# Performance work log

Measured on AMD Instinct MI355X. Metric: run time of the kernel, lower is better.

Reference implementation:

```python
import jax, jax.numpy as jnp
import numpy as np

C, B, D = 1_000_000, 4096, 128

def setup_inputs() -> dict:
    key = jax.random.key(0)
    ks = jax.random.split(key, 7)
    nodes = jax.random.normal(ks[0], (C, D), dtype=jnp.float32)
    z_local = jax.random.normal(ks[1], (B, D), dtype=jnp.float32)
    z_meta = jax.random.normal(ks[2], (D,), dtype=jnp.float32)
    # MLP params: Linear(3D -> D), GELU, Linear(D -> 1)
    W1 = jax.random.normal(ks[3], (3 * D, D), dtype=jnp.float32) / np.sqrt(3 * D)
    b1 = jnp.zeros((D,), dtype=jnp.float32)
    W2 = jax.random.normal(ks[4], (D, 1), dtype=jnp.float32) / np.sqrt(D)
    b2 = jnp.zeros((1,), dtype=jnp.float32)
    batch = jnp.sort(jax.random.randint(ks[5], (C,), 0, B, dtype=jnp.int64))
    return {"nodes": nodes, "z_local": z_local, "z_meta": z_meta,
            "W1": W1, "b1": b1, "W2": W2, "b2": b2, "batch": batch}

def reference(nodes, z_local, z_meta, W1, b1, W2, b2, batch):
    # gather per-graph global vector for each node, broadcast batch-wide meta
    z_local_tiled = z_local[batch]                       # [C, D]
    z_meta_tiled = jnp.broadcast_to(z_meta[None, :], nodes.shape)  # [C, D]
    combined = jnp.concatenate([nodes, z_local_tiled, z_meta_tiled], axis=-1)  # [C, 3D]
    h = jax.nn.gelu(combined @ W1 + b1, approximate=False)  # [C, D]
    logits = (h @ W2 + b2).squeeze(-1)                       # [C]
    return logits
```

## Files before the change

### kernel.cpp

```cpp
#include <hip/hip_runtime.h>
#include <hip/hip_bf16.h>


typedef __attribute__((ext_vector_type(8))) __bf16 bf16x8;
typedef __attribute__((ext_vector_type(4))) float f32x4;

#define D_DIM 128

__device__ __forceinline__ float gelu_exact(float x) {
    float t = 0.70710678118654752f * x;
    float a = fabsf(t);
    float d = __builtin_amdgcn_rcpf(fmaf(0.3275911f, a, 1.0f));
    float p = fmaf(1.061405429f, d, -1.453152027f);
    p = fmaf(p, d, 1.421413741f);
    p = fmaf(p, d, -0.284496736f);
    p = fmaf(p, d, 0.254829592f);
    p = p * d;
    float e = __builtin_amdgcn_exp2f(a * a * -1.4426950408889634f);
    float erf_a = fmaf(-p, e, 1.0f);
    float erf_t = copysignf(erf_a, t);
    return 0.5f * x * (1.0f + erf_t);
}

__global__ void prep_bias2(const float* __restrict__ z_meta, const float* __restrict__ W1,
                           const float* __restrict__ b1, float* __restrict__ bias2) {
    int n = threadIdx.x;
    float s = b1[n];
    for (int k = 0; k < D_DIM; ++k)
        s = fmaf(z_meta[k], W1[(2 * D_DIM + k) * D_DIM + n], s);
    bias2[n] = s;
}

__global__ void prep_w1f(const float* __restrict__ W1, __bf16* __restrict__ w1f) {
    int f = blockIdx.x * 256 + threadIdx.x;
    int j = f & 7, lane = (f >> 3) & 63, nt = (f >> 9) & 7, kc = f >> 12;
    int k = kc * 32 + (lane >> 4) * 8 + j;
    int n = nt * 16 + (lane & 15);
    w1f[f] = (__bf16)W1[k * D_DIM + n];
}

__global__ __launch_bounds__(128) void prep_pre(const float* __restrict__ z_local,
                                                const float* __restrict__ W1,
                                                const float* __restrict__ bias2,
                                                float* __restrict__ pre) {
    int n = threadIdx.x;
    int g0 = blockIdx.x * 8;
    float bz = bias2[n];
    float s[8];
#pragma unroll
    for (int g = 0; g < 8; ++g) s[g] = bz;
    for (int k = 0; k < D_DIM; ++k) {
        float wk = W1[(D_DIM + k) * D_DIM + n];
#pragma unroll
        for (int g = 0; g < 8; ++g)
            s[g] = fmaf(z_local[(size_t)(g0 + g) * D_DIM + k], wk, s[g]);
    }
#pragma unroll
    for (int g = 0; g < 8; ++g) pre[(size_t)(g0 + g) * D_DIM + n] = s[g];
}

__global__ __launch_bounds__(256) void readout_main(
    const float* __restrict__ nodes, const int* __restrict__ batch,
    const float* __restrict__ pre, const __bf16* __restrict__ w1f,
    const float* __restrict__ W2, const float* __restrict__ b2,
    float* __restrict__ out) {
    const int tid = threadIdx.x;
    const int wave = tid >> 6;
    const int lane = tid & 63;
    const int q = lane >> 4;
    const int c0 = lane & 15;
    const int row_base = blockIdx.x * 64 + wave * 16;

    const float* aptr = nodes + (size_t)(row_base + c0) * D_DIM + q * 8;
    f32x4 a[8];
#pragma unroll
    for (int kc = 0; kc < 4; ++kc) {
        a[2 * kc]     = *((const f32x4*)(aptr + kc * 32));
        a[2 * kc + 1] = *((const f32x4*)(aptr + kc * 32 + 4));
    }
    int brow[4];
#pragma unroll
    for (int r = 0; r < 4; ++r) brow[r] = batch[row_base + q * 4 + r];
    float w2v[8];
#pragma unroll
    for (int nt = 0; nt < 8; ++nt) w2v[nt] = W2[nt * 16 + c0];
    const float b2v = b2[0];

    f32x4 acc[8] = {};

    const bf16x8* bfr = (const bf16x8*)w1f;
#pragma unroll
    for (int kc = 0; kc < 4; ++kc) {
        bf16x8 af;
#pragma unroll
        for (int j = 0; j < 8; ++j)
            af[j] = (__bf16)a[2 * kc + (j >> 2)][j & 3];
#pragma unroll
        for (int nt = 0; nt < 8; ++nt) {
            bf16x8 bf = bfr[(kc * 8 + nt) * 64 + lane];
            acc[nt] = __builtin_amdgcn_mfma_f32_16x16x32_bf16(af, bf, acc[nt], 0, 0, 0);
        }
    }

#pragma unroll
    for (int r = 0; r < 4; ++r) {
        const float* prow = pre + (size_t)brow[r] * D_DIM;
        float partial = 0.f;
#pragma unroll
        for (int nt = 0; nt < 8; ++nt) {
            float u = acc[nt][r] + prow[nt * 16 + c0];
            partial += gelu_exact(u) * w2v[nt];
        }
        partial += __shfl_xor(partial, 1);
        partial += __shfl_xor(partial, 2);
        partial += __shfl_xor(partial, 4);
        partial += __shfl_xor(partial, 8);
        if (c0 == 0) out[row_base + q * 4 + r] = partial + b2v;
    }
}

extern "C" void kernel_launch(void* const* d_in, const int* in_sizes, int n_in,
                              void* d_out, int out_size, void* d_ws, size_t ws_size,
                              hipStream_t stream) {
    const float* nodes   = (const float*)d_in[0];
    const float* z_local = (const float*)d_in[1];
    const float* z_meta  = (const float*)d_in[2];
    const float* W1      = (const float*)d_in[3];
    const float* b1      = (const float*)d_in[4];
    const float* W2      = (const float*)d_in[5];
    const float* b2      = (const float*)d_in[6];
    const int*   batch   = (const int*)d_in[7];
    float* out = (float*)d_out;

    char* ws = (char*)d_ws;
    __bf16* w1f  = (__bf16*)ws;
    float* bias2 = (float*)(ws + 32768);
    float* pre   = (float*)(ws + 33280);

    prep_bias2<<<1, 128, 0, stream>>>(z_meta, W1, b1, bias2);
    prep_w1f<<<64, 256, 0, stream>>>(W1, w1f);
    prep_pre<<<512, 128, 0, stream>>>(z_local, W1, bias2, pre);

    readout_main<<<15625, 256, 0, stream>>>(nodes, batch, pre, w1f, W2, b2, out);
}
```

Baseline: 727.3 us.

## Fuse prep kernels into one launch and stage W1 fragments in LDS

Result: faster. 690.7 us (-5.0%).

```diff
diff --git a/kernel.cpp b/kernel.cpp
--- a/kernel.cpp
+++ b/kernel.cpp
@@ -1,9 +1,12 @@
 #include <hip/hip_runtime.h>
 #include <hip/hip_bf16.h>
+#include <cstdint>
 
 
 typedef __attribute__((ext_vector_type(8))) __bf16 bf16x8;
 typedef __attribute__((ext_vector_type(4))) float f32x4;
+typedef __attribute__((address_space(3))) uint32_t lds_u32;
+typedef __attribute__((address_space(1))) const uint32_t glob_u32;
 
 #define D_DIM 128
 
@@ -22,48 +25,48 @@
     return 0.5f * x * (1.0f + erf_t);
 }
 
-__global__ void prep_bias2(const float* __restrict__ z_meta, const float* __restrict__ W1,
-                           const float* __restrict__ b1, float* __restrict__ bias2) {
-    int n = threadIdx.x;
-    float s = b1[n];
-    for (int k = 0; k < D_DIM; ++k)
-        s = fmaf(z_meta[k], W1[(2 * D_DIM + k) * D_DIM + n], s);
-    bias2[n] = s;
-}
-
-__global__ void prep_w1f(const float* __restrict__ W1, __bf16* __restrict__ w1f) {
-    int f = blockIdx.x * 256 + threadIdx.x;
-    int j = f & 7, lane = (f >> 3) & 63, nt = (f >> 9) & 7, kc = f >> 12;
-    int k = kc * 32 + (lane >> 4) * 8 + j;
-    int n = nt * 16 + (lane & 15);
-    w1f[f] = (__bf16)W1[k * D_DIM + n];
-}
-
-__global__ __launch_bounds__(128) void prep_pre(const float* __restrict__ z_local,
-                                                const float* __restrict__ W1,
-                                                const float* __restrict__ bias2,
-                                                float* __restrict__ pre) {
-    int n = threadIdx.x;
-    int g0 = blockIdx.x * 8;
-    float bz = bias2[n];
-    float s[8];
+__global__ __launch_bounds__(256) void prep_all(
+    const float* __restrict__ z_local, const float* __restrict__ z_meta,
+    const float* __restrict__ W1, const float* __restrict__ b1,
+    __bf16* __restrict__ w1f, float* __restrict__ bias2, float* __restrict__ pre) {
+    const int blk = blockIdx.x;
+    const int tid = threadIdx.x;
+    if (blk < 64) {
+        int f = blk * 256 + tid;
+        int j = f & 7, lane = (f >> 3) & 63, nt = (f >> 9) & 7, kc = f >> 12;
+        int k = kc * 32 + (lane >> 4) * 8 + j;
+        int n = nt * 16 + (lane & 15);
+        w1f[f] = (__bf16)W1[k * D_DIM + n];
+    } else if (blk == 64) {
+        if (tid < D_DIM) {
+            int n = tid;
+            float s = b1[n];
+            for (int k = 0; k < D_DIM; ++k)
+                s = fmaf(z_meta[k], W1[(2 * D_DIM + k) * D_DIM + n], s);
+            bias2[n] = s;
+        }
+    } else {
+        int pb = blk - 65;
+        int n = tid & 127;
+        int g0 = pb * 8 + (tid >> 7) * 4;
+        float s[4] = {0.f, 0.f, 0.f, 0.f};
+        for (int k = 0; k < D_DIM; ++k) {
+            float wk = W1[(D_DIM + k) * D_DIM + n];
 #pragma unroll
-    for (int g = 0; g < 8; ++g) s[g] = bz;
-    for (int k = 0; k < D_DIM; ++k) {
-        float wk = W1[(D_DIM + k) * D_DIM + n];
+            for (int g = 0; g < 4; ++g)
+                s[g] = fmaf(z_local[(size_t)(g0 + g) * D_DIM + k], wk, s[g]);
+        }
 #pragma unroll
-        for (int g = 0; g < 8; ++g)
-            s[g] = fmaf(z_local[(size_t)(g0 + g) * D_DIM + k], wk, s[g]);
+        for (int g = 0; g < 4; ++g) pre[(size_t)(g0 + g) * D_DIM + n] = s[g];
     }
-#pragma unroll
-    for (int g = 0; g < 8; ++g) pre[(size_t)(g0 + g) * D_DIM + n] = s[g];
 }
 
 __global__ __launch_bounds__(256) void readout_main(
     const float* __restrict__ nodes, const int* __restrict__ batch,
     const float* __restrict__ pre, const __bf16* __restrict__ w1f,
-    const float* __restrict__ W2, const float* __restrict__ b2,
-    float* __restrict__ out) {
+    const float* __restrict__ bias2, const float* __restrict__ W2,
+    const float* __restrict__ b2, float* __restrict__ out) {
+    __shared__ __bf16 w1s[16384];
     const int tid = threadIdx.x;
     const int wave = tid >> 6;
     const int lane = tid & 63;
@@ -78,17 +81,33 @@
         a[2 * kc]     = *((const f32x4*)(aptr + kc * 32));
         a[2 * kc + 1] = *((const f32x4*)(aptr + kc * 32 + 4));
     }
+
+    {
+        const __bf16* gsrc = w1f + wave * 4096;
+        __bf16* ldst = w1s + wave * 4096;
+#pragma unroll
+        for (int it = 0; it < 8; ++it) {
+            __builtin_amdgcn_global_load_lds(
+                (glob_u32*)(gsrc + it * 512 + lane * 8),
+                (lds_u32*)(ldst + it * 512), 16, 0, 0);
+        }
+    }
+
     int brow[4];
 #pragma unroll
     for (int r = 0; r < 4; ++r) brow[r] = batch[row_base + q * 4 + r];
-    float w2v[8];
+    float w2v[8], bz[8];
 #pragma unroll
-    for (int nt = 0; nt < 8; ++nt) w2v[nt] = W2[nt * 16 + c0];
+    for (int nt = 0; nt < 8; ++nt) {
+        w2v[nt] = W2[nt * 16 + c0];
+        bz[nt]  = bias2[nt * 16 + c0];
+    }
     const float b2v = b2[0];
 
+    __syncthreads();
+
     f32x4 acc[8] = {};
-
-    const bf16x8* bfr = (const bf16x8*)w1f;
+    const bf16x8* bfr = (const bf16x8*)w1s;
 #pragma unroll
     for (int kc = 0; kc < 4; ++kc) {
         bf16x8 af;
@@ -108,7 +127,7 @@
         float partial = 0.f;
 #pragma unroll
         for (int nt = 0; nt < 8; ++nt) {
-            float u = acc[nt][r] + prow[nt * 16 + c0];
+            float u = acc[nt][r] + prow[nt * 16 + c0] + bz[nt];
             partial += gelu_exact(u) * w2v[nt];
         }
         partial += __shfl_xor(partial, 1);
@@ -137,9 +156,6 @@
     float* bias2 = (float*)(ws + 32768);
     float* pre   = (float*)(ws + 33280);
 
-    prep_bias2<<<1, 128, 0, stream>>>(z_meta, W1, b1, bias2);
-    prep_w1f<<<64, 256, 0, stream>>>(W1, w1f);
-    prep_pre<<<512, 128, 0, stream>>>(z_local, W1, bias2, pre);
-
-    readout_main<<<15625, 256, 0, stream>>>(nodes, batch, pre, w1f, W2, b2, out);
+    prep_all<<<577, 256, 0, stream>>>(z_local, z_meta, W1, b1, w1f, bias2, pre);
+    readout_main<<<15625, 256, 0, stream>>>(nodes, batch, pre, w1f, bias2, W2, b2, out);
 }
```
